# Kernel optimization log

Measured on AMD Instinct MI355X. Metric: run time of the kernel, lower is better.

The kernel has to match this reference:

```python
import jax, jax.numpy as jnp
import numpy as np

B, C, P = 8, 512, 4096
IC = C // 2  # inter_channels
EPS = 1e-5


def setup_inputs() -> dict:
    key = jax.random.key(0)
    ks = jax.random.split(key, 11)
    s_c = 1.0 / np.sqrt(C)
    s_2ic = 1.0 / np.sqrt(2 * IC)
    return {
        "x": jax.random.normal(ks[0], (B, C, P), dtype=jnp.float32),
        "w_theta": jax.random.uniform(ks[1], (IC, C), jnp.float32, -s_c, s_c),
        "b_theta": jax.random.uniform(ks[2], (IC,), jnp.float32, -s_c, s_c),
        "w_phi": jax.random.uniform(ks[3], (IC, C), jnp.float32, -s_c, s_c),
        "b_phi": jax.random.uniform(ks[4], (IC,), jnp.float32, -s_c, s_c),
        "w_g": jax.random.uniform(ks[5], (IC, C), jnp.float32, -s_c, s_c),
        "b_g": jax.random.uniform(ks[6], (IC,), jnp.float32, -s_c, s_c),
        "w_W": jax.random.uniform(ks[7], (C, 2 * IC), jnp.float32, -s_2ic, s_2ic),
        "b_W": jax.random.uniform(ks[8], (C,), jnp.float32, -s_2ic, s_2ic),
        "gamma": jax.random.normal(ks[9], (C,), dtype=jnp.float32),  # BN weight (nonzero so output is nontrivial)
        "beta": jax.random.normal(ks[10], (C,), dtype=jnp.float32),  # BN bias
    }


def reference(x, w_theta, b_theta, w_phi, b_phi, w_g, b_g, w_W, b_W, gamma, beta):
    # x: (b, c, p). key/value use batch rolled by one: cat([x[-1:], x[:-1]]).
    xr = jnp.roll(x, 1, axis=0)
    # 1x1 conv1d == per-point linear over channels
    q = jnp.einsum("oc,bcp->bpo", w_theta, x) + b_theta          # (b, p, ic)
    k = jnp.einsum("oc,bcp->bop", w_phi, xr) + b_phi[:, None]    # (b, ic, p)
    v = jnp.einsum("oc,bcp->bpo", w_g, xr) + b_g                 # (b, p, ic)
    f = jnp.einsum("bpi,bij->bpj", q, k)                         # (b, p, p)
    a = jax.nn.softmax(f, axis=-1)
    # fg_attention[b, j, :] = mean_i a[b, i, j], broadcast along the last dim.
    m = a.mean(axis=1)                                           # (b, p)
    # fg_attention @ value collapses exactly to outer(m, sum_p value):
    vsum = v.sum(axis=1)                                         # (b, ic)
    fg = m[:, :, None] * vsum[:, None, :]                        # (b, p, ic)
    bg = (1.0 - m)[:, :, None] * vsum[:, None, :]                # (b, p, ic)
    y = jnp.concatenate([fg, bg], axis=2)                        # (b, p, 2*ic)
    wy = jnp.einsum("oc,bpc->bop", w_W, y) + b_W[:, None]        # (b, c, p)
    # BatchNorm1d in training mode: biased batch stats over (batch, points)
    mu = wy.mean(axis=(0, 2), keepdims=True)
    var = ((wy - mu) ** 2).mean(axis=(0, 2), keepdims=True)
    wy = gamma[:, None] * (wy - mu) * jax.lax.rsqrt(var + EPS) + beta[:, None]
    return wy + x
```

## Files before the change

kernel.cpp:

```cpp
#include <hip/hip_runtime.h>

#define B_ 8
#define C_ 512
#define IC_ 256
#define P_ 4096
#define MSHIFT 44.0f

typedef unsigned short u16;
typedef short v8s __attribute__((ext_vector_type(8)));
typedef float v4f __attribute__((ext_vector_type(4)));

__device__ inline u16 f2bf(float f) {
    unsigned u = __float_as_uint(f);
    u += 0x7fffu + ((u >> 16) & 1u);
    return (u16)(u >> 16);
}

__global__ __launch_bounds__(256) void k_xsum(const float* __restrict__ x, float* __restrict__ Xsum) {
    int bc = blockIdx.x;
    const float* row = x + (size_t)bc * P_;
    float s = 0.f;
    for (int k = threadIdx.x * 4; k < P_; k += 256 * 4) {
        v4f v = *reinterpret_cast<const v4f*>(row + k);
        s += v.x + v.y + v.z + v.w;
    }
    for (int off = 1; off < 64; off <<= 1) s += __shfl_xor(s, off, 64);
    __shared__ float ps[4];
    if ((threadIdx.x & 63) == 0) ps[threadIdx.x >> 6] = s;
    __syncthreads();
    if (threadIdx.x == 0) Xsum[bc] = ps[0] + ps[1] + ps[2] + ps[3];
}

__global__ __launch_bounds__(256) void k_qk(const float* __restrict__ w, const float* __restrict__ bias,
                                            const float* __restrict__ x, u16* __restrict__ out, int roll) {
    __shared__ u16 w_lds[128 * 40];
    __shared__ u16 x_lds[128 * 40];
    const int tid = threadIdx.x;
    const int l = tid & 63;
    const int wv = tid >> 6;
    const int wo = (wv >> 1) * 64;
    const int wp = (wv & 1) * 64;
    const int p0 = blockIdx.x * 128;
    const int o0 = blockIdx.y * 128;
    const int b = blockIdx.z;
    const int bx = (b + roll) & 7;
    const float* xb = x + (size_t)bx * C_ * P_;

    v4f acc[4][4];
#pragma unroll
    for (int i = 0; i < 4; i++)
#pragma unroll
        for (int j = 0; j < 4; j++) { acc[i][j].x = 0.f; acc[i][j].y = 0.f; acc[i][j].z = 0.f; acc[i][j].w = 0.f; }

    for (int kc = 0; kc < C_; kc += 32) {
        __syncthreads();
#pragma unroll
        for (int it = 0; it < 4; ++it) {
            int flat = it * 256 + tid;
            int row = flat >> 3, ch = flat & 7;
            v4f wv4 = *reinterpret_cast<const v4f*>(w + (size_t)(o0 + row) * C_ + kc + ch * 4);
            uint2 pk;
            pk.x = f2bf(wv4.x) | ((unsigned)f2bf(wv4.y) << 16);
            pk.y = f2bf(wv4.z) | ((unsigned)f2bf(wv4.w) << 16);
            *reinterpret_cast<uint2*>(&w_lds[row * 40 + ch * 4]) = pk;
        }
#pragma unroll
        for (int it = 0; it < 4; ++it) {
            int flat = it * 256 + tid;
            int p = flat & 127;
            int cq = flat >> 7;
            const float* src = xb + (size_t)(kc + cq * 4) * P_ + p0 + p;
            float a0 = src[0], a1 = src[P_], a2 = src[2 * P_], a3 = src[3 * P_];
            uint2 pk;
            pk.x = f2bf(a0) | ((unsigned)f2bf(a1) << 16);
            pk.y = f2bf(a2) | ((unsigned)f2bf(a3) << 16);
            *reinterpret_cast<uint2*>(&x_lds[p * 40 + cq * 4]) = pk;
        }
        __syncthreads();
        v8s a[4];
#pragma unroll
        for (int mf = 0; mf < 4; ++mf)
            a[mf] = *reinterpret_cast<const v8s*>(&w_lds[(wo + mf * 16 + (l & 15)) * 40 + (l >> 4) * 8]);
#pragma unroll
        for (int nf = 0; nf < 4; ++nf) {
            v8s bf = *reinterpret_cast<const v8s*>(&x_lds[(wp + nf * 16 + (l & 15)) * 40 + (l >> 4) * 8]);
#pragma unroll
            for (int mf = 0; mf < 4; ++mf)
                acc[mf][nf] = __builtin_amdgcn_mfma_f32_16x16x32_bf16(a[mf], bf, acc[mf][nf], 0, 0, 0);
        }
    }
#pragma unroll
    for (int mf = 0; mf < 4; ++mf) {
        int ob = o0 + wo + mf * 16 + (l >> 4) * 4;
        v4f bi = *reinterpret_cast<const v4f*>(bias + ob);
#pragma unroll
        for (int nf = 0; nf < 4; ++nf) {
            int p = p0 + wp + nf * 16 + (l & 15);
            v4f v = acc[mf][nf];
            uint2 pk;
            pk.x = f2bf(v.x + bi.x) | ((unsigned)f2bf(v.y + bi.y) << 16);
            pk.y = f2bf(v.z + bi.z) | ((unsigned)f2bf(v.w + bi.w) << 16);
            *reinterpret_cast<uint2*>(&out[((size_t)b * P_ + p) * IC_ + ob]) = pk;
        }
    }
}

template <int PASS>
__global__ __launch_bounds__(256) void k_f(const u16* __restrict__ Q, const u16* __restrict__ K,
                                           float* __restrict__ srow, float* __restrict__ colsum) {
    __shared__ u16 K_lds[64 * 264];
    __shared__ float cp[4][64];
    const int tid = threadIdx.x;
    const int l = tid & 63;
    const int wv = tid >> 6;
    const int b = blockIdx.z;
    const int i0 = blockIdx.y * 128 + wv * 32;
    const int jbase = blockIdx.x * 2048;

    v8s a[2][8];
#pragma unroll
    for (int mf = 0; mf < 2; ++mf) {
        const u16* qrow = Q + ((size_t)b * P_ + i0 + mf * 16 + (l & 15)) * IC_ + (l >> 4) * 8;
#pragma unroll
        for (int s = 0; s < 8; ++s)
            a[mf][s] = *reinterpret_cast<const v8s*>(qrow + s * 32);
    }
    float racc[2][4];
    if (PASS == 1) {
#pragma unroll
        for (int mf = 0; mf < 2; ++mf)
#pragma unroll
            for (int r = 0; r < 4; ++r) racc[mf][r] = 0.f;
    } else {
#pragma unroll
        for (int mf = 0; mf < 2; ++mf)
#pragma unroll
            for (int r = 0; r < 4; ++r)
                racc[mf][r] = 1.0f / srow[(size_t)b * P_ + i0 + mf * 16 + (l >> 4) * 4 + r];
    }

    for (int t = 0; t < 32; ++t) {
        int j0 = jbase + t * 64;
        __syncthreads();
        if (PASS == 2 && t > 0 && tid < 64) {
            float sc = cp[0][tid] + cp[1][tid] + cp[2][tid] + cp[3][tid];
            atomicAdd(&colsum[(size_t)b * P_ + j0 - 64 + tid], sc);
        }
        {
            int r8 = tid >> 5, ch = tid & 31;
#pragma unroll
            for (int p8 = 0; p8 < 8; ++p8) {
                int row = p8 * 8 + r8;
                uint4 v = *reinterpret_cast<const uint4*>(K + ((size_t)b * P_ + j0 + row) * IC_ + ch * 8);
                *reinterpret_cast<uint4*>(&K_lds[row * 264 + ch * 8]) = v;
            }
        }
        __syncthreads();
        v4f acc[2][4];
#pragma unroll
        for (int mf = 0; mf < 2; ++mf)
#pragma unroll
            for (int nf = 0; nf < 4; ++nf) { acc[mf][nf].x = 0.f; acc[mf][nf].y = 0.f; acc[mf][nf].z = 0.f; acc[mf][nf].w = 0.f; }
#pragma unroll
        for (int s = 0; s < 8; ++s) {
#pragma unroll
            for (int nf = 0; nf < 4; ++nf) {
                v8s bf = *reinterpret_cast<const v8s*>(&K_lds[(nf * 16 + (l & 15)) * 264 + s * 32 + (l >> 4) * 8]);
                acc[0][nf] = __builtin_amdgcn_mfma_f32_16x16x32_bf16(a[0][s], bf, acc[0][nf], 0, 0, 0);
                acc[1][nf] = __builtin_amdgcn_mfma_f32_16x16x32_bf16(a[1][s], bf, acc[1][nf], 0, 0, 0);
            }
        }
        if (PASS == 1) {
#pragma unroll
            for (int mf = 0; mf < 2; ++mf) {
                float part[4] = {0.f, 0.f, 0.f, 0.f};
#pragma unroll
                for (int nf = 0; nf < 4; ++nf) {
                    part[0] += __expf(acc[mf][nf].x - MSHIFT);
                    part[1] += __expf(acc[mf][nf].y - MSHIFT);
                    part[2] += __expf(acc[mf][nf].z - MSHIFT);
                    part[3] += __expf(acc[mf][nf].w - MSHIFT);
                }
#pragma unroll
                for (int r = 0; r < 4; ++r) {
                    float v = part[r];
                    v += __shfl_xor(v, 1, 64);
                    v += __shfl_xor(v, 2, 64);
                    v += __shfl_xor(v, 4, 64);
                    v += __shfl_xor(v, 8, 64);
                    racc[mf][r] += v;
                }
            }
        } else {
            float c4[4];
#pragma unroll
            for (int nf = 0; nf < 4; ++nf) {
                float s_ = 0.f;
#pragma unroll
                for (int mf = 0; mf < 2; ++mf) {
                    s_ += __expf(acc[mf][nf].x - MSHIFT) * racc[mf][0];
                    s_ += __expf(acc[mf][nf].y - MSHIFT) * racc[mf][1];
                    s_ += __expf(acc[mf][nf].z - MSHIFT) * racc[mf][2];
                    s_ += __expf(acc[mf][nf].w - MSHIFT) * racc[mf][3];
                }
                s_ += __shfl_xor(s_, 16, 64);
                s_ += __shfl_xor(s_, 32, 64);
                c4[nf] = s_;
            }
            int g = l >> 4;
            float vout = (g == 0) ? c4[0] : ((g == 1) ? c4[1] : ((g == 2) ? c4[2] : c4[3]));
            cp[wv][l] = vout;
        }
    }
    __syncthreads();
    if (PASS == 2 && tid < 64) {
        float sc = cp[0][tid] + cp[1][tid] + cp[2][tid] + cp[3][tid];
        atomicAdd(&colsum[(size_t)b * P_ + jbase + 2048 - 64 + tid], sc);
    }
    if (PASS == 1 && (l & 15) == 0) {
#pragma unroll
        for (int mf = 0; mf < 2; ++mf)
#pragma unroll
            for (int r = 0; r < 4; ++r)
                atomicAdd(&srow[(size_t)b * P_ + i0 + mf * 16 + (l >> 4) * 4 + r], racc[mf][r]);
    }
}

__global__ __launch_bounds__(256) void k_vsum(const float* __restrict__ w_g, const float* __restrict__ b_g,
                                              const float* __restrict__ Xsum, float* __restrict__ vsum) {
    __shared__ float xs[C_];
    int b = blockIdx.x;
    int bp = (b + B_ - 1) & 7;
    for (int i = threadIdx.x; i < C_; i += 256) xs[i] = Xsum[bp * C_ + i];
    __syncthreads();
    int o = threadIdx.x;
    const float* wr = w_g + (size_t)o * C_;
    float acc = 0.f;
    for (int c = 0; c < C_; c += 4) {
        v4f wv = *reinterpret_cast<const v4f*>(wr + c);
        acc += wv.x * xs[c] + wv.y * xs[c + 1] + wv.z * xs[c + 2] + wv.w * xs[c + 3];
    }
    vsum[b * IC_ + o] = acc + (float)P_ * b_g[o];
}

__global__ __launch_bounds__(512) void k_kd(const float* __restrict__ w_W, const float* __restrict__ b_W,
                                            const float* __restrict__ vsum, float* __restrict__ Kv, float* __restrict__ Dv) {
    __shared__ float vs[IC_];
    int b = blockIdx.x;
    for (int i = threadIdx.x; i < IC_; i += 512) vs[i] = vsum[b * IC_ + i];
    __syncthreads();
    int o = threadIdx.x;
    const float* wr = w_W + (size_t)o * (2 * IC_);
    float a = 0.f, bv = 0.f;
    for (int ic = 0; ic < IC_; ic += 4) {
        v4f w1 = *reinterpret_cast<const v4f*>(wr + ic);
        v4f w2 = *reinterpret_cast<const v4f*>(wr + IC_ + ic);
        a += w1.x * vs[ic] + w1.y * vs[ic + 1] + w1.z * vs[ic + 2] + w1.w * vs[ic + 3];
        bv += w2.x * vs[ic] + w2.y * vs[ic + 1] + w2.z * vs[ic + 2] + w2.w * vs[ic + 3];
    }
    Kv[b * C_ + o] = bv + b_W[o];
    Dv[b * C_ + o] = a - bv;
}

__global__ __launch_bounds__(256) void k_s12(const float* __restrict__ colsum, float* __restrict__ s12) {
    int b = blockIdx.x;
    const float invP = 1.0f / P_;
    float s1 = 0.f, s2 = 0.f;
    for (int k = threadIdx.x * 4; k < P_; k += 1024) {
        v4f v = *reinterpret_cast<const v4f*>(colsum + (size_t)b * P_ + k);
        float m0 = v.x * invP, m1 = v.y * invP, m2 = v.z * invP, m3 = v.w * invP;
        s1 += m0 + m1 + m2 + m3;
        s2 += m0 * m0 + m1 * m1 + m2 * m2 + m3 * m3;
    }
    for (int off = 1; off < 64; off <<= 1) {
        s1 += __shfl_xor(s1, off, 64);
        s2 += __shfl_xor(s2, off, 64);
    }
    __shared__ float p1[4], p2[4];
    if ((threadIdx.x & 63) == 0) { p1[threadIdx.x >> 6] = s1; p2[threadIdx.x >> 6] = s2; }
    __syncthreads();
    if (threadIdx.x == 0) {
        s12[b * 2] = p1[0] + p1[1] + p1[2] + p1[3];
        s12[b * 2 + 1] = p2[0] + p2[1] + p2[2] + p2[3];
    }
}

__global__ __launch_bounds__(512) void k_bn(const float* __restrict__ Kv, const float* __restrict__ Dv,
                                            const float* __restrict__ s12, const float* __restrict__ gamma,
                                            const float* __restrict__ beta, float* __restrict__ alpha, float* __restrict__ ofs) {
    int o = threadIdx.x;
    const float invP = 1.0f / P_;
    float mu = 0.f, e2 = 0.f;
#pragma unroll
    for (int b = 0; b < B_; ++b) {
        float Kx = Kv[b * C_ + o], Dx = Dv[b * C_ + o];
        float m1 = s12[b * 2] * invP;
        float m2 = s12[b * 2 + 1] * invP;
        mu += Kx + Dx * m1;
        e2 += Kx * Kx + 2.f * Kx * Dx * m1 + Dx * Dx * m2;
    }
    mu *= 0.125f;
    e2 *= 0.125f;
    float var = e2 - mu * mu;
    float gi = gamma[o] * rsqrtf(var + 1e-5f);
    float bo = beta[o];
#pragma unroll
    for (int b = 0; b < B_; ++b) {
        alpha[b * C_ + o] = gi * Dv[b * C_ + o] * invP;
        ofs[b * C_ + o] = gi * (Kv[b * C_ + o] - mu) + bo;
    }
}

__global__ __launch_bounds__(256) void k_out(const float* __restrict__ x, const float* __restrict__ colsum,
                                             const float* __restrict__ alpha, const float* __restrict__ ofs,
                                             float* __restrict__ out) {
    int bo = blockIdx.x >> 2;
    int qd = blockIdx.x & 3;
    int b = bo >> 9;
    int p = qd * 1024 + threadIdx.x * 4;
    float al = alpha[bo], of = ofs[bo];
    size_t base = (size_t)bo * P_ + p;
    v4f xv = *reinterpret_cast<const v4f*>(x + base);
    v4f cs = *reinterpret_cast<const v4f*>(colsum + (size_t)b * P_ + p);
    v4f r;
    r.x = of + al * cs.x + xv.x;
    r.y = of + al * cs.y + xv.y;
    r.z = of + al * cs.z + xv.z;
    r.w = of + al * cs.w + xv.w;
    *reinterpret_cast<v4f*>(out + base) = r;
}

extern "C" void kernel_launch(void* const* d_in, const int* in_sizes, int n_in,
                              void* d_out, int out_size, void* d_ws, size_t ws_size,
                              hipStream_t stream) {
    const float* x = (const float*)d_in[0];
    const float* w_theta = (const float*)d_in[1];
    const float* b_theta = (const float*)d_in[2];
    const float* w_phi = (const float*)d_in[3];
    const float* b_phi = (const float*)d_in[4];
    const float* w_g = (const float*)d_in[5];
    const float* b_g = (const float*)d_in[6];
    const float* w_W = (const float*)d_in[7];
    const float* b_W = (const float*)d_in[8];
    const float* gamma = (const float*)d_in[9];
    const float* beta = (const float*)d_in[10];
    float* out = (float*)d_out;

    u16* Q = (u16*)d_ws;
    u16* K = Q + (size_t)B_ * P_ * IC_;
    float* fb = (float*)((char*)d_ws + (size_t)2 * B_ * P_ * IC_ * 2);
    float* srow = fb;
    float* colsum = srow + B_ * P_;
    float* Xsum = colsum + B_ * P_;
    float* vsum = Xsum + B_ * C_;
    float* Kv = vsum + B_ * IC_;
    float* Dv = Kv + B_ * C_;
    float* s12 = Dv + B_ * C_;
    float* alpha = s12 + 16;
    float* ofs = alpha + B_ * C_;

    hipMemsetAsync(srow, 0, sizeof(float) * 2 * B_ * P_, stream);
    k_xsum<<<B_ * C_, 256, 0, stream>>>(x, Xsum);
    k_qk<<<dim3(32, 2, 8), 256, 0, stream>>>(w_theta, b_theta, x, Q, 0);
    k_qk<<<dim3(32, 2, 8), 256, 0, stream>>>(w_phi, b_phi, x, K, B_ - 1);
    k_vsum<<<B_, 256, 0, stream>>>(w_g, b_g, Xsum, vsum);
    k_kd<<<B_, 512, 0, stream>>>(w_W, b_W, vsum, Kv, Dv);
    k_f<1><<<dim3(2, 32, 8), 256, 0, stream>>>(Q, K, srow, colsum);
    k_f<2><<<dim3(2, 32, 8), 256, 0, stream>>>(Q, K, srow, colsum);
    k_s12<<<B_, 256, 0, stream>>>(colsum, s12);
    k_bn<<<1, 512, 0, stream>>>(Kv, Dv, s12, gamma, beta, alpha, ofs);
    k_out<<<B_ * C_ * 4, 256, 0, stream>>>(x, colsum, alpha, ofs, out);
}
```

Before: 475.5 us.

## Double-buffer K via direct global-to-LDS loads, enlarge attention tiles, merge QK launches

The attention-score kernels now give each wave 64 query rows instead of 32. K tiles are staged with global_load_lds into two swizzled LDS buffers, so the next tile loads while MFMAs run on the current one. The grid block index is remapped to group blocks of the same batch, and the row-sum shuffle reduction moves out of the loop to the end. Separately, the two Q/K projection launches are merged into one grid, and the output kernel handles a whole row per block. The larger tiles cut K reloads and add register pressure, with occupancy pinned by a launch bound of 2 blocks.

```diff
diff --git a/kernel.cpp b/kernel.cpp
--- a/kernel.cpp
+++ b/kernel.cpp
@@ -14,6 +14,12 @@
     unsigned u = __float_as_uint(f);
     u += 0x7fffu + ((u >> 16) & 1u);
     return (u16)(u >> 16);
+}
+
+typedef const __attribute__((address_space(1))) unsigned int* gp1_t;
+typedef __attribute__((address_space(3))) unsigned int* lp3_t;
+__device__ inline void gload_lds16(const void* g, void* l) {
+    __builtin_amdgcn_global_load_lds((gp1_t)g, (lp3_t)l, 16, 0, 0);
 }
 
 __global__ __launch_bounds__(256) void k_xsum(const float* __restrict__ x, float* __restrict__ Xsum) {
@@ -31,8 +37,9 @@
     if (threadIdx.x == 0) Xsum[bc] = ps[0] + ps[1] + ps[2] + ps[3];
 }
 
-__global__ __launch_bounds__(256) void k_qk(const float* __restrict__ w, const float* __restrict__ bias,
-                                            const float* __restrict__ x, u16* __restrict__ out, int roll) {
+__global__ __launch_bounds__(256) void k_qk(const float* __restrict__ w_theta, const float* __restrict__ b_theta,
+                                            const float* __restrict__ w_phi, const float* __restrict__ b_phi,
+                                            const float* __restrict__ x, u16* __restrict__ Q, u16* __restrict__ K) {
     __shared__ u16 w_lds[128 * 40];
     __shared__ u16 x_lds[128 * 40];
     const int tid = threadIdx.x;
@@ -42,8 +49,13 @@
     const int wp = (wv & 1) * 64;
     const int p0 = blockIdx.x * 128;
     const int o0 = blockIdx.y * 128;
-    const int b = blockIdx.z;
-    const int bx = (b + roll) & 7;
+    const int z = blockIdx.z;
+    const int which = z >> 3;
+    const int b = z & 7;
+    const float* w = which ? w_phi : w_theta;
+    const float* bias = which ? b_phi : b_theta;
+    u16* out = which ? K : Q;
+    const int bx = which ? ((b + 7) & 7) : b;
     const float* xb = x + (size_t)bx * C_ * P_;
 
     v4f acc[4][4];
@@ -106,90 +118,102 @@
 }
 
 template <int PASS>
-__global__ __launch_bounds__(256) void k_f(const u16* __restrict__ Q, const u16* __restrict__ K,
-                                           float* __restrict__ srow, float* __restrict__ colsum) {
-    __shared__ u16 K_lds[64 * 264];
-    __shared__ float cp[4][64];
+__global__ __launch_bounds__(256, 2) void k_f(const u16* __restrict__ Q, const u16* __restrict__ K,
+                                              float* __restrict__ srow, float* __restrict__ colsum) {
+    __shared__ __align__(16) unsigned char smem[65536 + 2048];
+    float* cp = (float*)(smem + 65536);
     const int tid = threadIdx.x;
     const int l = tid & 63;
     const int wv = tid >> 6;
-    const int b = blockIdx.z;
-    const int i0 = blockIdx.y * 128 + wv * 32;
-    const int jbase = blockIdx.x * 2048;
-
-    v8s a[2][8];
-#pragma unroll
-    for (int mf = 0; mf < 2; ++mf) {
+    int lin = blockIdx.x + blockIdx.y * 4 + blockIdx.z * 64;
+    int nlin = (lin & 7) * 64 + (lin >> 3);
+    const int jchunk = nlin & 3;
+    const int yb = (nlin >> 2) & 15;
+    const int b = nlin >> 6;
+    const int i0 = yb * 256 + wv * 64;
+    const int jbase = jchunk * 1024;
+    const u16* Kb = K + (size_t)b * P_ * IC_;
+
+    v8s a[4][8];
+#pragma unroll
+    for (int mf = 0; mf < 4; ++mf) {
         const u16* qrow = Q + ((size_t)b * P_ + i0 + mf * 16 + (l & 15)) * IC_ + (l >> 4) * 8;
 #pragma unroll
         for (int s = 0; s < 8; ++s)
             a[mf][s] = *reinterpret_cast<const v8s*>(qrow + s * 32);
     }
-    float racc[2][4];
+    float racc[4][4];
     if (PASS == 1) {
 #pragma unroll
-        for (int mf = 0; mf < 2; ++mf)
+        for (int mf = 0; mf < 4; ++mf)
 #pragma unroll
             for (int r = 0; r < 4; ++r) racc[mf][r] = 0.f;
     } else {
 #pragma unroll
-        for (int mf = 0; mf < 2; ++mf)
-#pragma unroll
-            for (int r = 0; r < 4; ++r)
-                racc[mf][r] = 1.0f / srow[(size_t)b * P_ + i0 + mf * 16 + (l >> 4) * 4 + r];
-    }
-
-    for (int t = 0; t < 32; ++t) {
+        for (int mf = 0; mf < 4; ++mf) {
+            v4f sr = *reinterpret_cast<const v4f*>(&srow[(size_t)b * P_ + i0 + mf * 16 + (l >> 4) * 4]);
+            racc[mf][0] = 1.0f / sr.x;
+            racc[mf][1] = 1.0f / sr.y;
+            racc[mf][2] = 1.0f / sr.z;
+            racc[mf][3] = 1.0f / sr.w;
+        }
+    }
+
+    auto stage = [&](int t, int bufsel) {
         int j0 = jbase + t * 64;
-        __syncthreads();
+#pragma unroll
+        for (int it = 0; it < 8; ++it) {
+            int slot = wv * 8192 + it * 1024 + (l << 4);
+            int row = slot >> 9;
+            int brg = (slot & 511) ^ ((row & 7) << 4);
+            const unsigned char* g = (const unsigned char*)(Kb + (size_t)(j0 + row) * IC_) + brg;
+            gload_lds16(g, smem + bufsel * 32768 + wv * 8192 + it * 1024);
+        }
+    };
+
+    stage(0, 0);
+    asm volatile("s_waitcnt vmcnt(0)" ::: "memory");
+    __syncthreads();
+    int cur = 0;
+    for (int t = 0; t < 16; ++t) {
+        if (t < 15) stage(t + 1, cur ^ 1);
         if (PASS == 2 && t > 0 && tid < 64) {
-            float sc = cp[0][tid] + cp[1][tid] + cp[2][tid] + cp[3][tid];
-            atomicAdd(&colsum[(size_t)b * P_ + j0 - 64 + tid], sc);
-        }
-        {
-            int r8 = tid >> 5, ch = tid & 31;
-#pragma unroll
-            for (int p8 = 0; p8 < 8; ++p8) {
-                int row = p8 * 8 + r8;
-                uint4 v = *reinterpret_cast<const uint4*>(K + ((size_t)b * P_ + j0 + row) * IC_ + ch * 8);
-                *reinterpret_cast<uint4*>(&K_lds[row * 264 + ch * 8]) = v;
+            float* cpp = cp + ((t - 1) & 1) * 256;
+            float sc = cpp[tid] + cpp[64 + tid] + cpp[128 + tid] + cpp[192 + tid];
+            atomicAdd(&colsum[(size_t)b * P_ + jbase + (t - 1) * 64 + tid], sc);
+        }
+        v4f acc[4][4];
+#pragma unroll
+        for (int mf = 0; mf < 4; ++mf)
+#pragma unroll
+            for (int nf = 0; nf < 4; ++nf) { acc[mf][nf].x = 0.f; acc[mf][nf].y = 0.f; acc[mf][nf].z = 0.f; acc[mf][nf].w = 0.f; }
+#pragma unroll
+        for (int s = 0; s < 8; ++s) {
+#pragma unroll
+            for (int nf = 0; nf < 4; ++nf) {
+                int row = nf * 16 + (l & 15);
+                int byte_ = cur * 32768 + row * 512 + ((s * 64 + (l >> 4) * 16) ^ ((row & 7) << 4));
+                v8s bf = *reinterpret_cast<const v8s*>(smem + byte_);
+#pragma unroll
+                for (int mf = 0; mf < 4; ++mf)
+                    acc[mf][nf] = __builtin_amdgcn_mfma_f32_16x16x32_bf16(a[mf][s], bf, acc[mf][nf], 0, 0, 0);
             }
         }
-        __syncthreads();
-        v4f acc[2][4];
-#pragma unroll
-        for (int mf = 0; mf < 2; ++mf)
-#pragma unroll
-            for (int nf = 0; nf < 4; ++nf) { acc[mf][nf].x = 0.f; acc[mf][nf].y = 0.f; acc[mf][nf].z = 0.f; acc[mf][nf].w = 0.f; }
-#pragma unroll
-        for (int s = 0; s < 8; ++s) {
-#pragma unroll
-            for (int nf = 0; nf < 4; ++nf) {
-                v8s bf = *reinterpret_cast<const v8s*>(&K_lds[(nf * 16 + (l & 15)) * 264 + s * 32 + (l >> 4) * 8]);
-                acc[0][nf] = __builtin_amdgcn_mfma_f32_16x16x32_bf16(a[0][s], bf, acc[0][nf], 0, 0, 0);
-                acc[1][nf] = __builtin_amdgcn_mfma_f32_16x16x32_bf16(a[1][s], bf, acc[1][nf], 0, 0, 0);
-            }
-        }
         if (PASS == 1) {
 #pragma unroll
-            for (int mf = 0; mf < 2; ++mf) {
-                float part[4] = {0.f, 0.f, 0.f, 0.f};
+            for (int mf = 0; mf < 4; ++mf) {
+                float p0 = 0.f, p1 = 0.f, p2 = 0.f, p3 = 0.f;
 #pragma unroll
                 for (int nf = 0; nf < 4; ++nf) {
-                    part[0] += __expf(acc[mf][nf].x - MSHIFT);
-                    part[1] += __expf(acc[mf][nf].y - MSHIFT);
-                    part[2] += __expf(acc[mf][nf].z - MSHIFT);
-                    part[3] += __expf(acc[mf][nf].w - MSHIFT);
+                    p0 += __expf(acc[mf][nf].x - MSHIFT);
+                    p1 += __expf(acc[mf][nf].y - MSHIFT);
+                    p2 += __expf(acc[mf][nf].z - MSHIFT);
+                    p3 += __expf(acc[mf][nf].w - MSHIFT);
                 }
-#pragma unroll
-                for (int r = 0; r < 4; ++r) {
-                    float v = part[r];
-                    v += __shfl_xor(v, 1, 64);
-                    v += __shfl_xor(v, 2, 64);
-                    v += __shfl_xor(v, 4, 64);
-                    v += __shfl_xor(v, 8, 64);
-                    racc[mf][r] += v;
-                }
+                racc[mf][0] += p0;
+                racc[mf][1] += p1;
+                racc[mf][2] += p2;
+                racc[mf][3] += p3;
             }
         } else {
             float c4[4];
@@ -197,7 +221,7 @@
             for (int nf = 0; nf < 4; ++nf) {
                 float s_ = 0.f;
 #pragma unroll
-                for (int mf = 0; mf < 2; ++mf) {
+                for (int mf = 0; mf < 4; ++mf) {
                     s_ += __expf(acc[mf][nf].x - MSHIFT) * racc[mf][0];
                     s_ += __expf(acc[mf][nf].y - MSHIFT) * racc[mf][1];
                     s_ += __expf(acc[mf][nf].z - MSHIFT) * racc[mf][2];
@@ -209,20 +233,30 @@
             }
             int g = l >> 4;
             float vout = (g == 0) ? c4[0] : ((g == 1) ? c4[1] : ((g == 2) ? c4[2] : c4[3]));
-            cp[wv][l] = vout;
-        }
-    }
-    __syncthreads();
+            cp[(t & 1) * 256 + wv * 64 + l] = vout;
+        }
+        asm volatile("s_waitcnt vmcnt(0)" ::: "memory");
+        __syncthreads();
+        cur ^= 1;
+    }
     if (PASS == 2 && tid < 64) {
-        float sc = cp[0][tid] + cp[1][tid] + cp[2][tid] + cp[3][tid];
-        atomicAdd(&colsum[(size_t)b * P_ + jbase + 2048 - 64 + tid], sc);
-    }
-    if (PASS == 1 && (l & 15) == 0) {
-#pragma unroll
-        for (int mf = 0; mf < 2; ++mf)
-#pragma unroll
-            for (int r = 0; r < 4; ++r)
-                atomicAdd(&srow[(size_t)b * P_ + i0 + mf * 16 + (l >> 4) * 4 + r], racc[mf][r]);
+        float* cpp = cp + 256;
+        float sc = cpp[tid] + cpp[64 + tid] + cpp[128 + tid] + cpp[192 + tid];
+        atomicAdd(&colsum[(size_t)b * P_ + jbase + 15 * 64 + tid], sc);
+    }
+    if (PASS == 1) {
+#pragma unroll
+        for (int mf = 0; mf < 4; ++mf)
+#pragma unroll
+            for (int r = 0; r < 4; ++r) {
+                float v = racc[mf][r];
+                v += __shfl_xor(v, 1, 64);
+                v += __shfl_xor(v, 2, 64);
+                v += __shfl_xor(v, 4, 64);
+                v += __shfl_xor(v, 8, 64);
+                if ((l & 15) == 0)
+                    atomicAdd(&srow[(size_t)b * P_ + i0 + mf * 16 + (l >> 4) * 4 + r], v);
+            }
     }
 }
 
@@ -314,20 +348,23 @@
 __global__ __launch_bounds__(256) void k_out(const float* __restrict__ x, const float* __restrict__ colsum,
                                              const float* __restrict__ alpha, const float* __restrict__ ofs,
                                              float* __restrict__ out) {
-    int bo = blockIdx.x >> 2;
-    int qd = blockIdx.x & 3;
+    int bo = blockIdx.x;
     int b = bo >> 9;
-    int p = qd * 1024 + threadIdx.x * 4;
     float al = alpha[bo], of = ofs[bo];
-    size_t base = (size_t)bo * P_ + p;
-    v4f xv = *reinterpret_cast<const v4f*>(x + base);
-    v4f cs = *reinterpret_cast<const v4f*>(colsum + (size_t)b * P_ + p);
-    v4f r;
-    r.x = of + al * cs.x + xv.x;
-    r.y = of + al * cs.y + xv.y;
-    r.z = of + al * cs.z + xv.z;
-    r.w = of + al * cs.w + xv.w;
-    *reinterpret_cast<v4f*>(out + base) = r;
+    size_t base = (size_t)bo * P_;
+    const float* cb = colsum + (size_t)b * P_;
+#pragma unroll
+    for (int q = 0; q < 4; ++q) {
+        int p = q * 1024 + threadIdx.x * 4;
+        v4f xv = *reinterpret_cast<const v4f*>(x + base + p);
+        v4f cs = *reinterpret_cast<const v4f*>(cb + p);
+        v4f r;
+        r.x = of + al * cs.x + xv.x;
+        r.y = of + al * cs.y + xv.y;
+        r.z = of + al * cs.z + xv.z;
+        r.w = of + al * cs.w + xv.w;
+        *reinterpret_cast<v4f*>(out + base + p) = r;
+    }
 }
 
 extern "C" void kernel_launch(void* const* d_in, const int* in_sizes, int n_in,
@@ -361,13 +398,12 @@
 
     hipMemsetAsync(srow, 0, sizeof(float) * 2 * B_ * P_, stream);
     k_xsum<<<B_ * C_, 256, 0, stream>>>(x, Xsum);
-    k_qk<<<dim3(32, 2, 8), 256, 0, stream>>>(w_theta, b_theta, x, Q, 0);
-    k_qk<<<dim3(32, 2, 8), 256, 0, stream>>>(w_phi, b_phi, x, K, B_ - 1);
+    k_qk<<<dim3(32, 2, 16), 256, 0, stream>>>(w_theta, b_theta, w_phi, b_phi, x, Q, K);
     k_vsum<<<B_, 256, 0, stream>>>(w_g, b_g, Xsum, vsum);
     k_kd<<<B_, 512, 0, stream>>>(w_W, b_W, vsum, Kv, Dv);
-    k_f<1><<<dim3(2, 32, 8), 256, 0, stream>>>(Q, K, srow, colsum);
-    k_f<2><<<dim3(2, 32, 8), 256, 0, stream>>>(Q, K, srow, colsum);
+    k_f<1><<<dim3(4, 16, 8), 256, 0, stream>>>(Q, K, srow, colsum);
+    k_f<2><<<dim3(4, 16, 8), 256, 0, stream>>>(Q, K, srow, colsum);
     k_s12<<<B_, 256, 0, stream>>>(colsum, s12);
     k_bn<<<1, 512, 0, stream>>>(Kv, Dv, s12, gamma, beta, alpha, ofs);
-    k_out<<<B_ * C_ * 4, 256, 0, stream>>>(x, colsum, alpha, ofs, out);
-}
+    k_out<<<B_ * C_, 256, 0, stream>>>(x, colsum, alpha, ofs, out);
+}
```

After: 419.6 us. 1.13x faster.
